# Optimization experiments

Measured on AMD Instinct MI355X. Metric: run time of the kernel, lower is better.

## Reference

```python
import jax, jax.numpy as jnp
import numpy as np

EPS = 1e-5

def _bn_eval(x, gamma, beta, mu, var):
    # channelwise BN (eval mode) on [B,C,N,K]
    inv = gamma / jnp.sqrt(var + EPS)
    return x * inv[None, :, None, None] + (beta - mu * inv)[None, :, None, None]

def _gather_nk(x, idx):
    # x: [B,C,N], idx: [B,N,K] -> [B,C,N,K]
    return jnp.take_along_axis(x[:, :, None, :], idx[:, None, :, :], axis=3)

def setup_inputs() -> dict:
    key = jax.random.key(0)
    ks = jax.random.split(key, 20)
    B, N, K, C = 2, 16384, 16, 128
    s = 0.05
    inp = {
        'coord': jax.random.normal(ks[0], (B, N, 3), jnp.float32),
        'feature_spa': jax.random.normal(ks[1], (B, C, N), jnp.float32),
        'feature_spe': jax.random.normal(ks[2], (B, C, N), jnp.float32),
        'neighbor_indices': jax.random.randint(ks[3], (B, N, K), 0, N),
        'wq': jax.random.normal(ks[4], (C, C), jnp.float32) * s,
        'wk': jax.random.normal(ks[5], (C, C), jnp.float32) * s,
        'wv_w': jax.random.normal(ks[6], (C, C), jnp.float32) * s,
        'wv_b': jax.random.normal(ks[7], (C,), jnp.float32) * s,
        'pos_w1': jax.random.normal(ks[8], (3, 3), jnp.float32) * 0.3,
        'pos_b1': jax.random.normal(ks[9], (3,), jnp.float32) * 0.1,
        'pos_g': jnp.ones((3,), jnp.float32),
        'pos_beta': jnp.zeros((3,), jnp.float32),
        'pos_mu': jnp.zeros((3,), jnp.float32),
        'pos_var': jnp.ones((3,), jnp.float32),
        'pos_w2': jax.random.normal(ks[10], (1, 3), jnp.float32) * 0.3,
        'pos_b2': jax.random.normal(ks[11], (1,), jnp.float32) * 0.1,
        'sc_w1': jax.random.normal(ks[12], (2, 2), jnp.float32) * 0.3,
        'sc_b1': jax.random.normal(ks[13], (2,), jnp.float32) * 0.1,
        'sc_g': jnp.ones((2,), jnp.float32),
        'sc_beta': jnp.zeros((2,), jnp.float32),
        'sc_mu': jnp.zeros((2,), jnp.float32),
        'sc_var': jnp.ones((2,), jnp.float32),
        'sc_w2': jax.random.normal(ks[14], (1, 2), jnp.float32) * 0.3,
        'sc_b2': jax.random.normal(ks[15], (1,), jnp.float32) * 0.1,
    }
    return inp

def reference(coord, feature_spa, feature_spe, neighbor_indices,
              wq, wk, wv_w, wv_b,
              pos_w1, pos_b1, pos_g, pos_beta, pos_mu, pos_var, pos_w2, pos_b2,
              sc_w1, sc_b1, sc_g, sc_beta, sc_mu, sc_var, sc_w2, sc_b2):
    C = feature_spa.shape[1]
    coord_t = jnp.transpose(coord, (0, 2, 1))                      # [B,3,N]
    Q = jnp.einsum('oc,bcn->bon', wq, feature_spa)                 # [B,C,N]
    Kf = jnp.einsum('oc,bcn->bon', wk, feature_spe)
    V = jnp.einsum('oc,bcn->bon', wv_w, feature_spe) + wv_b[None, :, None]
    # positional branch
    neighbor_coord = _gather_nk(coord_t, neighbor_indices)         # [B,3,N,K]
    coord_diff = neighbor_coord - coord_t[:, :, :, None]
    g = jnp.exp(-2.0 * coord_diff ** 2)                            # [B,3,N,K]
    h = jnp.einsum('oc,bcnk->bonk', pos_w1, g) + pos_b1[None, :, None, None]
    h = jax.nn.relu(_bn_eval(h, pos_g, pos_beta, pos_mu, pos_var))
    scores_coord = jnp.einsum('oc,bcnk->bonk', pos_w2, h) + pos_b2[None, :, None, None]  # [B,1,N,K]
    # feature branch
    Kg = _gather_nk(Kf, neighbor_indices)                          # [B,C,N,K]
    Vg = _gather_nk(V, neighbor_indices)                           # [B,C,N,K]
    scores_feat = jnp.einsum('bcn,bcnk->bnk', Q, Kg) / np.sqrt(C)  # [B,N,K]
    scores = jnp.concatenate([scores_coord, scores_feat[:, None]], axis=1)  # [B,2,N,K]
    s = jnp.einsum('oc,bcnk->bonk', sc_w1, scores) + sc_b1[None, :, None, None]
    s = jax.nn.relu(_bn_eval(s, sc_g, sc_beta, sc_mu, sc_var))
    s = jnp.einsum('oc,bcnk->bonk', sc_w2, s) + sc_b2[None, :, None, None]  # [B,1,N,K]
    attn = jax.nn.softmax(s, axis=-1)                              # [B,1,N,K]
    fusion_feat = jnp.sum(attn * Vg, axis=-1)                      # [B,C,N]
    return fusion_feat
```

## Files before the change

kernel.cpp:

```cpp
#include <hip/hip_runtime.h>
#include <cstdint>
#include <cstddef>

#define B_ 2
#define N_ 16384
#define K_ 16
#define C_ 128

typedef __attribute__((ext_vector_type(8))) short  bf16x8;
typedef __attribute__((ext_vector_type(4))) float  f32x4;

__device__ __forceinline__ float bfu_lo(uint32_t w) { return __uint_as_float(w << 16); }
__device__ __forceinline__ float bfu_hi(uint32_t w) { return __uint_as_float(w & 0xffff0000u); }

__device__ __forceinline__ ushort f32_to_bf16_rne(float x) {
    uint32_t u = __float_as_uint(x);
    u += 0x7FFFu + ((u >> 16) & 1u);
    return (ushort)(u >> 16);
}
__device__ __forceinline__ uint32_t pack_bf16x2(float lo, float hi) {
    return (uint32_t)f32_to_bf16_rne(lo) | ((uint32_t)f32_to_bf16_rne(hi) << 16);
}

__device__ __forceinline__ uint32_t e5m2_enc(float x) {
    union { _Float16 h; ushort u; } cv;
    cv.h = (_Float16)x;
    ushort h = (ushort)(cv.u + 0x7Fu + ((cv.u >> 8) & 1u));
    return (uint32_t)(h >> 8) & 0xFFu;
}
__device__ __forceinline__ float e5m2_dec(uint32_t byteval) {
    union { _Float16 h; ushort u; } cv;
    cv.u = (ushort)(byteval << 8);
    return (float)cv.h;
}

__device__ __forceinline__ int xswz(int row, int c) {
    return row * 128 + ((((c >> 3) ^ (row & 7)) << 3) | (c & 7));
}

__global__ __launch_bounds__(512) void qkv_gemm(
    const float* __restrict__ spa, const float* __restrict__ spe,
    const float* __restrict__ wq, const float* __restrict__ wk,
    const float* __restrict__ wv, const float* __restrict__ wvb,
    ushort* __restrict__ Qt16, uint8_t* __restrict__ Kt8, ushort* __restrict__ Vt16)
{
    const int nt    = blockIdx.x * 128;
    const int b     = blockIdx.y;
    const int which = blockIdx.z;
    const float* X = (which == 0) ? spa : spe;
    const float* W = (which == 0) ? wq : (which == 1 ? wk : wv);

    __shared__ ushort xs[128 * 128];
    __shared__ ushort ws[128 * 128];

    const int t    = threadIdx.x;
    const int w    = t >> 6;
    const int lane = t & 63;
    const int l15  = lane & 15;
    const int l4   = lane >> 4;
    const int ow   = (w & 3) * 32;
    const int nw   = (w >> 2) * 64;

    {
        const int r  = t >> 2;
        const int c0 = (t & 3) * 32;
        const float* srcw = W + r * C_ + c0;
        #pragma unroll
        for (int q = 0; q < 4; ++q) {
            float4 a  = *(const float4*)(srcw + q * 8);
            float4 b4 = *(const float4*)(srcw + q * 8 + 4);
            uint4 pk;
            pk.x = pack_bf16x2(a.x, a.y);
            pk.y = pack_bf16x2(a.z, a.w);
            pk.z = pack_bf16x2(b4.x, b4.y);
            pk.w = pack_bf16x2(b4.z, b4.w);
            *(uint4*)&ws[xswz(r, c0 + q * 8)] = pk;
        }
    }
    {
        const int c  = t >> 2;
        const int nq = (t & 3) * 32;
        const float* xrow = X + ((size_t)b * C_ + c) * N_ + nt + nq;
        #pragma unroll
        for (int q = 0; q < 8; ++q) {
            float4 v = ((const float4*)xrow)[q];
            const int n = nq + q * 4;
            xs[xswz(n + 0, c)] = f32_to_bf16_rne(v.x);
            xs[xswz(n + 1, c)] = f32_to_bf16_rne(v.y);
            xs[xswz(n + 2, c)] = f32_to_bf16_rne(v.z);
            xs[xswz(n + 3, c)] = f32_to_bf16_rne(v.w);
        }
    }
    __syncthreads();

    f32x4 acc[2][4];
    #pragma unroll
    for (int of = 0; of < 2; ++of)
        #pragma unroll
        for (int nf = 0; nf < 4; ++nf)
            acc[of][nf] = (f32x4){0.f, 0.f, 0.f, 0.f};

    #pragma unroll
    for (int kc = 0; kc < 4; ++kc) {
        const int cb = kc * 32 + l4 * 8;
        bf16x8 afr[2];
        #pragma unroll
        for (int of = 0; of < 2; ++of)
            afr[of] = *(__shared__ bf16x8*)&ws[xswz(ow + of * 16 + l15, cb)];
        bf16x8 bfr[4];
        #pragma unroll
        for (int nf = 0; nf < 4; ++nf)
            bfr[nf] = *(__shared__ bf16x8*)&xs[xswz(nw + nf * 16 + l15, cb)];
        #pragma unroll
        for (int of = 0; of < 2; ++of)
            #pragma unroll
            for (int nf = 0; nf < 4; ++nf)
                acc[of][nf] = __builtin_amdgcn_mfma_f32_16x16x32_bf16(
                    afr[of], bfr[nf], acc[of][nf], 0, 0, 0);
    }

    #pragma unroll
    for (int of = 0; of < 2; ++of) {
        const int o0r = ow + of * 16 + l4 * 4;
        if (which == 1) {
            #pragma unroll
            for (int nf = 0; nf < 4; ++nf) {
                const int n = nt + nw + nf * 16 + l15;
                uint32_t w8 = e5m2_enc(acc[of][nf][0])
                            | (e5m2_enc(acc[of][nf][1]) << 8)
                            | (e5m2_enc(acc[of][nf][2]) << 16)
                            | (e5m2_enc(acc[of][nf][3]) << 24);
                *(uint32_t*)(Kt8 + ((size_t)b * N_ + n) * C_ + o0r) = w8;
            }
        } else {
            ushort* Out = (which == 0) ? Qt16 : Vt16;
            float4 bv = make_float4(0.f, 0.f, 0.f, 0.f);
            if (which == 2) bv = *(const float4*)(wvb + o0r);
            #pragma unroll
            for (int nf = 0; nf < 4; ++nf) {
                const int n = nt + nw + nf * 16 + l15;
                uint2 pk;
                pk.x = pack_bf16x2(acc[of][nf][0] + bv.x, acc[of][nf][1] + bv.y);
                pk.y = pack_bf16x2(acc[of][nf][2] + bv.z, acc[of][nf][3] + bv.w);
                *(uint2*)(Out + ((size_t)b * N_ + n) * C_ + o0r) = pk;
            }
        }
    }
}

struct GR {
    uint4    ka, kb;
    uint32_t vv[16];
    float    nc0, nc1, nc2;
};

__device__ __forceinline__ void gather_issue(
    GR& g2, const int (*idx_s)[16], int nl, int b,
    const uint8_t* __restrict__ Kt8, const ushort* __restrict__ Vt16,
    const float* __restrict__ coord, int gk, int sub, int lane)
{
    const int idxg = idx_s[nl][gk];
    const uint4* kp = (const uint4*)(Kt8 + ((size_t)(b * N_ + idxg)) * C_ + sub * 32);
    g2.ka = kp[0];
    g2.kb = kp[1];
    #pragma unroll
    for (int k = 0; k < 16; ++k) {
        const int vid = idx_s[nl][k];
        g2.vv[k] = ((const uint32_t*)(Vt16 + ((size_t)(b * N_ + vid)) * C_))[lane];
    }
    const float* ncp = coord + ((size_t)(b * N_ + idxg)) * 3;
    g2.nc0 = ncp[0];
    g2.nc1 = ncp[1];
    g2.nc2 = ncp[2];
}

__global__ __launch_bounds__(256) void attn_fuse(
    const float* __restrict__ coord, const int* __restrict__ nbr,
    const ushort* __restrict__ Qt16, const uint8_t* __restrict__ Kt8,
    const ushort* __restrict__ Vt16,
    const float* __restrict__ pw1, const float* __restrict__ pb1,
    const float* __restrict__ pg,  const float* __restrict__ pbeta,
    const float* __restrict__ pmu, const float* __restrict__ pvar,
    const float* __restrict__ pw2, const float* __restrict__ pb2,
    const float* __restrict__ sw1, const float* __restrict__ sb1,
    const float* __restrict__ sg,  const float* __restrict__ sbeta,
    const float* __restrict__ smu, const float* __restrict__ svar,
    const float* __restrict__ sw2, const float* __restrict__ sb2,
    float* __restrict__ out)
{
    const int bid  = blockIdx.x;
    const int b    = bid >> 10;
    const int n0   = (bid & 1023) << 4;
    const int t    = threadIdx.x;
    const int w    = t >> 6;
    const int lane = t & 63;
    const int g    = lane >> 2;
    const int sub  = lane & 3;

    __shared__ float qs[16][132];
    __shared__ int   idx_s[16][16];
    __shared__ float cs[16][3];
    __shared__ float ot[128][17];

    {
        const int n = t >> 4, c0 = (t & 15) * 8;
        uint4 qw = *(const uint4*)(Qt16 + ((size_t)(b * N_ + n0 + n)) * C_ + c0);
        qs[n][c0 + 0] = bfu_lo(qw.x); qs[n][c0 + 1] = bfu_hi(qw.x);
        qs[n][c0 + 2] = bfu_lo(qw.y); qs[n][c0 + 3] = bfu_hi(qw.y);
        qs[n][c0 + 4] = bfu_lo(qw.z); qs[n][c0 + 5] = bfu_hi(qw.z);
        qs[n][c0 + 6] = bfu_lo(qw.w); qs[n][c0 + 7] = bfu_hi(qw.w);
        idx_s[t >> 4][t & 15] = nbr[((size_t)(b * N_ + n0 + (t >> 4))) * K_ + (t & 15)];
        if (t < 48) cs[t / 3][t % 3] = coord[((size_t)(b * N_ + n0 + t / 3)) * 3 + (t % 3)];
    }
    __syncthreads();

    float pinv[3], pofs[3], w1r[3][3], w2r[3], pb1r[3];
    #pragma unroll
    for (int o = 0; o < 3; ++o) {
        float inv = pg[o] / sqrtf(pvar[o] + 1e-5f);
        pinv[o] = inv;
        pofs[o] = pbeta[o] - pmu[o] * inv;
        pb1r[o] = pb1[o];
        w2r[o]  = pw2[o];
        #pragma unroll
        for (int i2 = 0; i2 < 3; ++i2) w1r[o][i2] = pw1[o * 3 + i2];
    }
    const float pb2v = pb2[0];
    float sinv[2], sofs[2], sb1r[2];
    #pragma unroll
    for (int o = 0; o < 2; ++o) {
        float inv = sg[o] / sqrtf(svar[o] + 1e-5f);
        sinv[o] = inv;
        sofs[o] = sbeta[o] - smu[o] * inv;
        sb1r[o] = sb1[o];
    }
    const float sw1r[4] = {sw1[0], sw1[1], sw1[2], sw1[3]};
    const float sw2r[2] = {sw2[0], sw2[1]};
    const float sb2v = sb2[0];
    const float inv_sqrtC = 0.088388347648318447f;

    auto compute = [&](int nl, GR& gr) {
        const float* qrow = &qs[nl][sub * 32];
        float acc = 0.f;
        {
            const uint32_t wds[8] = {gr.ka.x, gr.ka.y, gr.ka.z, gr.ka.w,
                                     gr.kb.x, gr.kb.y, gr.kb.z, gr.kb.w};
            #pragma unroll
            for (int j = 0; j < 8; ++j) {
                const uint32_t ww = wds[j];
                acc = fmaf(qrow[j * 4 + 0], e5m2_dec(ww & 0xffu), acc);
                acc = fmaf(qrow[j * 4 + 1], e5m2_dec((ww >> 8) & 0xffu), acc);
                acc = fmaf(qrow[j * 4 + 2], e5m2_dec((ww >> 16) & 0xffu), acc);
                acc = fmaf(qrow[j * 4 + 3], e5m2_dec(ww >> 24), acc);
            }
        }
        acc += __shfl_xor(acc, 1);
        acc += __shfl_xor(acc, 2);
        const float sfeat = acc * inv_sqrtC;

        float d0 = gr.nc0 - cs[nl][0], d1 = gr.nc1 - cs[nl][1], d2 = gr.nc2 - cs[nl][2];
        float g0 = expf(-2.f * d0 * d0);
        float g1 = expf(-2.f * d1 * d1);
        float g2 = expf(-2.f * d2 * d2);
        float h0 = fmaf(w1r[0][0], g0, fmaf(w1r[0][1], g1, fmaf(w1r[0][2], g2, pb1r[0])));
        float h1 = fmaf(w1r[1][0], g0, fmaf(w1r[1][1], g1, fmaf(w1r[1][2], g2, pb1r[1])));
        float h2 = fmaf(w1r[2][0], g0, fmaf(w1r[2][1], g1, fmaf(w1r[2][2], g2, pb1r[2])));
        h0 = fmaxf(fmaf(h0, pinv[0], pofs[0]), 0.f);
        h1 = fmaxf(fmaf(h1, pinv[1], pofs[1]), 0.f);
        h2 = fmaxf(fmaf(h2, pinv[2], pofs[2]), 0.f);
        const float scoord = fmaf(w2r[0], h0, fmaf(w2r[1], h1, fmaf(w2r[2], h2, pb2v)));

        float t0 = fmaf(sw1r[0], scoord, fmaf(sw1r[1], sfeat, sb1r[0]));
        t0 = fmaxf(fmaf(t0, sinv[0], sofs[0]), 0.f);
        float t1 = fmaf(sw1r[2], scoord, fmaf(sw1r[3], sfeat, sb1r[1]));
        t1 = fmaxf(fmaf(t1, sinv[1], sofs[1]), 0.f);
        float s = fmaf(sw2r[0], t0, fmaf(sw2r[1], t1, sb2v));

        float m = s;
        m = fmaxf(m, __shfl_xor(m, 4));
        m = fmaxf(m, __shfl_xor(m, 8));
        m = fmaxf(m, __shfl_xor(m, 16));
        m = fmaxf(m, __shfl_xor(m, 32));
        float e = expf(s - m);
        float den = e;
        den += __shfl_xor(den, 4);
        den += __shfl_xor(den, 8);
        den += __shfl_xor(den, 16);
        den += __shfl_xor(den, 32);
        const float attn = e / den;

        float a0 = 0.f, a1 = 0.f;
        #pragma unroll
        for (int k = 0; k < 16; ++k) {
            const float ak = __shfl(attn, k << 2);
            a0 = fmaf(ak, bfu_lo(gr.vv[k]), a0);
            a1 = fmaf(ak, bfu_hi(gr.vv[k]), a1);
        }
        ot[2 * lane][nl]     = a0;
        ot[2 * lane + 1][nl] = a1;
    };

    GR A, B;
    gather_issue(A, idx_s, w * 4 + 0, b, Kt8, Vt16, coord, g, sub, lane);
    gather_issue(B, idx_s, w * 4 + 1, b, Kt8, Vt16, coord, g, sub, lane);
    compute(w * 4 + 0, A);
    gather_issue(A, idx_s, w * 4 + 2, b, Kt8, Vt16, coord, g, sub, lane);
    compute(w * 4 + 1, B);
    gather_issue(B, idx_s, w * 4 + 3, b, Kt8, Vt16, coord, g, sub, lane);
    compute(w * 4 + 2, A);
    compute(w * 4 + 3, B);

    __syncthreads();

    {
        const int col = t & 15;
        const int r0  = (t >> 4) * 8;
        #pragma unroll
        for (int r = 0; r < 8; ++r)
            out[((size_t)(b * C_ + r0 + r)) * N_ + n0 + col] = ot[r0 + r][col];
    }
}

extern "C" void kernel_launch(void* const* d_in, const int* in_sizes, int n_in,
                              void* d_out, int out_size, void* d_ws, size_t ws_size,
                              hipStream_t stream) {
    const float* coord = (const float*)d_in[0];
    const float* spa   = (const float*)d_in[1];
    const float* spe   = (const float*)d_in[2];
    const int*   nbr   = (const int*)  d_in[3];
    const float* wq    = (const float*)d_in[4];
    const float* wk    = (const float*)d_in[5];
    const float* wv    = (const float*)d_in[6];
    const float* wvb   = (const float*)d_in[7];
    const float* pw1   = (const float*)d_in[8];
    const float* pb1   = (const float*)d_in[9];
    const float* pg    = (const float*)d_in[10];
    const float* pbeta = (const float*)d_in[11];
    const float* pmu   = (const float*)d_in[12];
    const float* pvar  = (const float*)d_in[13];
    const float* pw2   = (const float*)d_in[14];
    const float* pb2   = (const float*)d_in[15];
    const float* sw1   = (const float*)d_in[16];
    const float* sb1   = (const float*)d_in[17];
    const float* sg    = (const float*)d_in[18];
    const float* sbeta = (const float*)d_in[19];
    const float* smu   = (const float*)d_in[20];
    const float* svar  = (const float*)d_in[21];
    const float* sw2   = (const float*)d_in[22];
    const float* sb2   = (const float*)d_in[23];
    float* out = (float*)d_out;

    ushort*  Qt16 = (ushort*)d_ws;
    ushort*  Vt16 = Qt16 + (size_t)B_ * N_ * C_;
    uint8_t* Kt8  = (uint8_t*)(Vt16 + (size_t)B_ * N_ * C_);

    qkv_gemm<<<dim3(N_ / 128, B_, 3), 512, 0, stream>>>(
        spa, spe, wq, wk, wv, wvb, Qt16, Kt8, Vt16);

    attn_fuse<<<dim3(B_ * N_ / 16), 256, 0, stream>>>(
        coord, nbr, Qt16, Kt8, Vt16,
        pw1, pb1, pg, pbeta, pmu, pvar, pw2, pb2,
        sw1, sb1, sg, sbeta, smu, svar, sw2, sb2,
        out);
}
```

Baseline: 169.5 us.

## Fuse K and V projections sharing the spe tile; load weights into registers

The QKV GEMM grid drops from three z-slices to two, so the block handling feature_spe computes both the K and V projections from a single shared-memory copy of the input tile. This avoids reading and converting feature_spe twice. Weight fragments now go from global memory straight into registers as bf16 instead of being staged through a shared-memory tile, which removes that LDS buffer. In exchange the K/V block holds twice the accumulators and weight fragments, which raises register pressure and can lower occupancy, and the Q and K/V blocks now do unequal amounts of work.

```diff
diff --git a/kernel.cpp b/kernel.cpp
--- a/kernel.cpp
+++ b/kernel.cpp
@@ -44,14 +44,12 @@
     const float* __restrict__ wv, const float* __restrict__ wvb,
     ushort* __restrict__ Qt16, uint8_t* __restrict__ Kt8, ushort* __restrict__ Vt16)
 {
-    const int nt    = blockIdx.x * 128;
-    const int b     = blockIdx.y;
-    const int which = blockIdx.z;
-    const float* X = (which == 0) ? spa : spe;
-    const float* W = (which == 0) ? wq : (which == 1 ? wk : wv);
+    const int nt  = blockIdx.x * 128;
+    const int b   = blockIdx.y;
+    const bool isQ = (blockIdx.z == 0);
+    const float* X = isQ ? spa : spe;
 
     __shared__ ushort xs[128 * 128];
-    __shared__ ushort ws[128 * 128];
 
     const int t    = threadIdx.x;
     const int w    = t >> 6;
@@ -62,22 +60,6 @@
     const int nw   = (w >> 2) * 64;
 
     {
-        const int r  = t >> 2;
-        const int c0 = (t & 3) * 32;
-        const float* srcw = W + r * C_ + c0;
-        #pragma unroll
-        for (int q = 0; q < 4; ++q) {
-            float4 a  = *(const float4*)(srcw + q * 8);
-            float4 b4 = *(const float4*)(srcw + q * 8 + 4);
-            uint4 pk;
-            pk.x = pack_bf16x2(a.x, a.y);
-            pk.y = pack_bf16x2(a.z, a.w);
-            pk.z = pack_bf16x2(b4.x, b4.y);
-            pk.w = pack_bf16x2(b4.z, b4.w);
-            *(uint4*)&ws[xswz(r, c0 + q * 8)] = pk;
-        }
-    }
-    {
         const int c  = t >> 2;
         const int nq = (t & 3) * 32;
         const float* xrow = X + ((size_t)b * C_ + c) * N_ + nt + nq;
@@ -91,58 +73,117 @@
             xs[xswz(n + 3, c)] = f32_to_bf16_rne(v.w);
         }
     }
-    __syncthreads();
-
-    f32x4 acc[2][4];
-    #pragma unroll
-    for (int of = 0; of < 2; ++of)
-        #pragma unroll
-        for (int nf = 0; nf < 4; ++nf)
-            acc[of][nf] = (f32x4){0.f, 0.f, 0.f, 0.f};
-
-    #pragma unroll
-    for (int kc = 0; kc < 4; ++kc) {
-        const int cb = kc * 32 + l4 * 8;
-        bf16x8 afr[2];
+
+    auto load_wfrags = [&](const float* __restrict__ W, bf16x8 wf[2][4]) {
+        #pragma unroll
+        for (int of = 0; of < 2; ++of) {
+            #pragma unroll
+            for (int kc = 0; kc < 4; ++kc) {
+                const float* wp = W + (size_t)(ow + of * 16 + l15) * C_ + kc * 32 + l4 * 8;
+                float4 a  = *(const float4*)wp;
+                float4 b4 = *(const float4*)(wp + 4);
+                bf16x8 f;
+                f[0] = (short)f32_to_bf16_rne(a.x);
+                f[1] = (short)f32_to_bf16_rne(a.y);
+                f[2] = (short)f32_to_bf16_rne(a.z);
+                f[3] = (short)f32_to_bf16_rne(a.w);
+                f[4] = (short)f32_to_bf16_rne(b4.x);
+                f[5] = (short)f32_to_bf16_rne(b4.y);
+                f[6] = (short)f32_to_bf16_rne(b4.z);
+                f[7] = (short)f32_to_bf16_rne(b4.w);
+                wf[of][kc] = f;
+            }
+        }
+    };
+
+    if (isQ) {
+        bf16x8 wfq[2][4];
+        load_wfrags(wq, wfq);
+        __syncthreads();
+
+        f32x4 acc[2][4];
         #pragma unroll
         for (int of = 0; of < 2; ++of)
-            afr[of] = *(__shared__ bf16x8*)&ws[xswz(ow + of * 16 + l15, cb)];
-        bf16x8 bfr[4];
-        #pragma unroll
-        for (int nf = 0; nf < 4; ++nf)
-            bfr[nf] = *(__shared__ bf16x8*)&xs[xswz(nw + nf * 16 + l15, cb)];
-        #pragma unroll
-        for (int of = 0; of < 2; ++of)
             #pragma unroll
             for (int nf = 0; nf < 4; ++nf)
-                acc[of][nf] = __builtin_amdgcn_mfma_f32_16x16x32_bf16(
-                    afr[of], bfr[nf], acc[of][nf], 0, 0, 0);
-    }
-
-    #pragma unroll
-    for (int of = 0; of < 2; ++of) {
-        const int o0r = ow + of * 16 + l4 * 4;
-        if (which == 1) {
-            #pragma unroll
-            for (int nf = 0; nf < 4; ++nf) {
-                const int n = nt + nw + nf * 16 + l15;
-                uint32_t w8 = e5m2_enc(acc[of][nf][0])
-                            | (e5m2_enc(acc[of][nf][1]) << 8)
-                            | (e5m2_enc(acc[of][nf][2]) << 16)
-                            | (e5m2_enc(acc[of][nf][3]) << 24);
-                *(uint32_t*)(Kt8 + ((size_t)b * N_ + n) * C_ + o0r) = w8;
-            }
-        } else {
-            ushort* Out = (which == 0) ? Qt16 : Vt16;
-            float4 bv = make_float4(0.f, 0.f, 0.f, 0.f);
-            if (which == 2) bv = *(const float4*)(wvb + o0r);
+                acc[of][nf] = (f32x4){0.f, 0.f, 0.f, 0.f};
+
+        #pragma unroll
+        for (int kc = 0; kc < 4; ++kc) {
+            const int cb = kc * 32 + l4 * 8;
+            bf16x8 bfr[4];
+            #pragma unroll
+            for (int nf = 0; nf < 4; ++nf)
+                bfr[nf] = *(__shared__ bf16x8*)&xs[xswz(nw + nf * 16 + l15, cb)];
+            #pragma unroll
+            for (int of = 0; of < 2; ++of)
+                #pragma unroll
+                for (int nf = 0; nf < 4; ++nf)
+                    acc[of][nf] = __builtin_amdgcn_mfma_f32_16x16x32_bf16(
+                        wfq[of][kc], bfr[nf], acc[of][nf], 0, 0, 0);
+        }
+
+        #pragma unroll
+        for (int of = 0; of < 2; ++of) {
+            const int o0r = ow + of * 16 + l4 * 4;
             #pragma unroll
             for (int nf = 0; nf < 4; ++nf) {
                 const int n = nt + nw + nf * 16 + l15;
                 uint2 pk;
-                pk.x = pack_bf16x2(acc[of][nf][0] + bv.x, acc[of][nf][1] + bv.y);
-                pk.y = pack_bf16x2(acc[of][nf][2] + bv.z, acc[of][nf][3] + bv.w);
-                *(uint2*)(Out + ((size_t)b * N_ + n) * C_ + o0r) = pk;
+                pk.x = pack_bf16x2(acc[of][nf][0], acc[of][nf][1]);
+                pk.y = pack_bf16x2(acc[of][nf][2], acc[of][nf][3]);
+                *(uint2*)(Qt16 + ((size_t)b * N_ + n) * C_ + o0r) = pk;
+            }
+        }
+    } else {
+        bf16x8 wfk[2][4], wfv[2][4];
+        load_wfrags(wk, wfk);
+        load_wfrags(wv, wfv);
+        __syncthreads();
+
+        f32x4 acck[2][4], accv[2][4];
+        #pragma unroll
+        for (int of = 0; of < 2; ++of)
+            #pragma unroll
+            for (int nf = 0; nf < 4; ++nf) {
+                acck[of][nf] = (f32x4){0.f, 0.f, 0.f, 0.f};
+                accv[of][nf] = (f32x4){0.f, 0.f, 0.f, 0.f};
+            }
+
+        #pragma unroll
+        for (int kc = 0; kc < 4; ++kc) {
+            const int cb = kc * 32 + l4 * 8;
+            bf16x8 bfr[4];
+            #pragma unroll
+            for (int nf = 0; nf < 4; ++nf)
+                bfr[nf] = *(__shared__ bf16x8*)&xs[xswz(nw + nf * 16 + l15, cb)];
+            #pragma unroll
+            for (int of = 0; of < 2; ++of)
+                #pragma unroll
+                for (int nf = 0; nf < 4; ++nf) {
+                    acck[of][nf] = __builtin_amdgcn_mfma_f32_16x16x32_bf16(
+                        wfk[of][kc], bfr[nf], acck[of][nf], 0, 0, 0);
+                    accv[of][nf] = __builtin_amdgcn_mfma_f32_16x16x32_bf16(
+                        wfv[of][kc], bfr[nf], accv[of][nf], 0, 0, 0);
+                }
+        }
+
+        #pragma unroll
+        for (int of = 0; of < 2; ++of) {
+            const int o0r = ow + of * 16 + l4 * 4;
+            const float4 bv = *(const float4*)(wvb + o0r);
+            #pragma unroll
+            for (int nf = 0; nf < 4; ++nf) {
+                const int n = nt + nw + nf * 16 + l15;
+                uint32_t w8 = e5m2_enc(acck[of][nf][0])
+                            | (e5m2_enc(acck[of][nf][1]) << 8)
+                            | (e5m2_enc(acck[of][nf][2]) << 16)
+                            | (e5m2_enc(acck[of][nf][3]) << 24);
+                *(uint32_t*)(Kt8 + ((size_t)b * N_ + n) * C_ + o0r) = w8;
+                uint2 pk;
+                pk.x = pack_bf16x2(accv[of][nf][0] + bv.x, accv[of][nf][1] + bv.y);
+                pk.y = pack_bf16x2(accv[of][nf][2] + bv.z, accv[of][nf][3] + bv.w);
+                *(uint2*)(Vt16 + ((size_t)b * N_ + n) * C_ + o0r) = pk;
             }
         }
     }
@@ -354,7 +395,7 @@
     ushort*  Vt16 = Qt16 + (size_t)B_ * N_ * C_;
     uint8_t* Kt8  = (uint8_t*)(Vt16 + (size_t)B_ * N_ * C_);
 
-    qkv_gemm<<<dim3(N_ / 128, B_, 3), 512, 0, stream>>>(
+    qkv_gemm<<<dim3(N_ / 128, B_, 2), 512, 0, stream>>>(
         spa, spe, wq, wk, wv, wvb, Qt16, Kt8, Vt16);
 
     attn_fuse<<<dim3(B_ * N_ / 16), 256, 0, stream>>>(
```

Result: slower. 173.1 us (+2.1%).
